# Kernel tuning notes

Measured on AMD Instinct MI355X. Metric: run time of the kernel, lower is better.

The kernel has to match this reference:

```python
import jax, jax.numpy as jnp
import numpy as np

B, T, D = 32, 2048, 128


def setup_inputs() -> dict:
    key = jax.random.key(0)
    k1, k2, k3 = jax.random.split(key, 3)
    values = jax.random.normal(k1, (B, T, D), dtype=jnp.float32)
    # monotonically increasing per-feature timestamps (irregular sampling)
    times = jnp.cumsum(jax.random.uniform(k2, (B, T, D), dtype=jnp.float32), axis=1)
    mask = jax.random.randint(k3, (B, T, D), 0, 2) > 0  # True = observed
    return {"values": values, "times": times, "mask": mask}


def _fill(x, t, mask):
    """Parallel forward fill (LOCF) and backward fill (NOCB) of x and t.

    Replaces the serial Keras RNN scan with cummax/cummin over observation
    indices followed by a gather. Matches ForwardCell semantics:
      forward : x init 0, t init times[:, 0, :]
      backward: x init 0, t init max(times, axis=1)
    """
    Tn = x.shape[1]
    ar = jnp.broadcast_to(jnp.arange(Tn, dtype=jnp.int32)[None, :, None], x.shape)
    # ---- forward fill ----
    fidx = jax.lax.cummax(jnp.where(mask, ar, -1), axis=1)  # last observed idx
    fvalid = fidx >= 0
    fi = jnp.clip(fidx, 0, Tn - 1)
    x_last = jnp.where(fvalid, jnp.take_along_axis(x, fi, axis=1), 0.0)
    t_last = jnp.where(fvalid, jnp.take_along_axis(t, fi, axis=1), t[:, :1, :])
    # ---- backward fill ----
    bidx = jax.lax.cummin(jnp.where(mask, ar, Tn), axis=1, reverse=True)  # next observed idx
    bvalid = bidx < Tn
    bi = jnp.clip(bidx, 0, Tn - 1)
    x_next = jnp.where(bvalid, jnp.take_along_axis(x, bi, axis=1), 0.0)
    t_next = jnp.where(bvalid, jnp.take_along_axis(t, bi, axis=1),
                       jnp.max(t, axis=1, keepdims=True))
    return x_last, t_last, x_next, t_next


def reference(values, times, mask):
    x_last, t_last, x_next, t_next = _fill(values, times, mask)
    denom = t_next - t_last
    num = x_last * (t_next - times) + x_next * (times - t_last)
    safe = denom != 0.0
    x_itp = num / jnp.where(safe, denom, 1.0)
    x_itp = jnp.where(safe & jnp.isfinite(x_itp), x_itp, 0.0)  # nan/inf -> 0
    return jnp.where(mask, values, x_itp)
```

## Files before the change

### kernel.cpp

```cpp
#include <hip/hip_runtime.h>
#include <math.h>

constexpr int B   = 32;
constexpr int T   = 2048;
constexpr int D   = 128;
constexpr int TB  = 32;
constexpr int W   = 8;
constexpr int RT  = TB + 2 * W;
constexpr int RG  = 8;
constexpr int RPT = RT / RG;
constexpr int DGN = 32;
constexpr int NT  = T / TB;

__global__ __launch_bounds__(256)
void linterp_kernel(const float* __restrict__ values,
                    const float* __restrict__ times,
                    const int*   __restrict__ mask,
                    float*       __restrict__ out)
{
    __shared__ float sFX[RG][D];
    __shared__ float sFT[RG][D];
    __shared__ float sBX[RG][D];
    __shared__ float sBT[RG][D];

    const int tid  = threadIdx.x;
    const int dg   = tid & (DGN - 1);
    const int rg   = tid >> 5;
    const int tile = blockIdx.x & (NT - 1);
    const int b    = blockIdx.x >> 6;
    const int d    = dg * 4;
    const int base = b * T * D + d;
    const int tlo  = tile * TB;
    const int row0 = tlo - W + rg * RPT;

    float4 v[RPT], tv[RPT];
    unsigned int mb[4] = {0u, 0u, 0u, 0u};
#pragma unroll
    for (int i = 0; i < RPT; ++i) {
        const int r = row0 + i;
        if (r >= 0 && r < T) {
            const int off = base + r * D;
            v[i]  = *(const float4*)(values + off);
            tv[i] = *(const float4*)(times + off);
            const int4 m = *(const int4*)(mask + off);
            mb[0] |= (m.x != 0 ? 1u : 0u) << i;
            mb[1] |= (m.y != 0 ? 1u : 0u) << i;
            mb[2] |= (m.z != 0 ? 1u : 0u) << i;
            mb[3] |= (m.w != 0 ? 1u : 0u) << i;
        } else {
            v[i]  = make_float4(0.f, 0.f, 0.f, 0.f);
            tv[i] = make_float4(0.f, 0.f, 0.f, 0.f);
        }
    }

    const float4 tf4 = *(const float4*)(times + base);
    const float4 te4 = *(const float4*)(times + base + (T - 1) * D);

    {
        float fX[4], fT[4], bX[4], bT[4];
#pragma unroll
        for (int j = 0; j < 4; ++j) { fX[j] = 0.f; fT[j] = -1.f; bX[j] = 0.f; bT[j] = -1.f; }
#pragma unroll
        for (int i = 0; i < RPT; ++i) {
            const float* xp = (const float*)&v[i];
            const float* tp = (const float*)&tv[i];
#pragma unroll
            for (int j = 0; j < 4; ++j) {
                if ((mb[j] >> i) & 1u) {
                    fX[j] = xp[j]; fT[j] = tp[j];
                    if (bT[j] < 0.f) { bX[j] = xp[j]; bT[j] = tp[j]; }
                }
            }
        }
        *(float4*)&sFX[rg][d] = make_float4(fX[0], fX[1], fX[2], fX[3]);
        *(float4*)&sFT[rg][d] = make_float4(fT[0], fT[1], fT[2], fT[3]);
        *(float4*)&sBX[rg][d] = make_float4(bX[0], bX[1], bX[2], bX[3]);
        *(float4*)&sBT[rg][d] = make_float4(bT[0], bT[1], bT[2], bT[3]);
    }
    __syncthreads();

    const bool has_out = (rg >= 1) && (rg <= 6);

    float cfX[4], cfT[4], cbX[4], cbT[4];
#pragma unroll
    for (int j = 0; j < 4; ++j) { cfX[j] = 0.f; cfT[j] = -1.f; cbX[j] = 0.f; cbT[j] = -1.f; }

    if (has_out) {
        for (int r2 = 0; r2 < rg; ++r2) {
            const float4 px = *(const float4*)&sFX[r2][d];
            const float4 pt = *(const float4*)&sFT[r2][d];
            const float* pxp = (const float*)&px;
            const float* ptp = (const float*)&pt;
#pragma unroll
            for (int j = 0; j < 4; ++j)
                if (ptp[j] >= 0.f) { cfX[j] = pxp[j]; cfT[j] = ptp[j]; }
        }
        for (int r2 = RG - 1; r2 > rg; --r2) {
            const float4 nx = *(const float4*)&sBX[r2][d];
            const float4 nt = *(const float4*)&sBT[r2][d];
            const float* nxp = (const float*)&nx;
            const float* ntp = (const float*)&nt;
#pragma unroll
            for (int j = 0; j < 4; ++j)
                if (ntp[j] >= 0.f) { cbX[j] = nxp[j]; cbT[j] = ntp[j]; }
        }

#pragma unroll
        for (int j = 0; j < 4; ++j) {
            if (cfT[j] < 0.f) {
                for (int r = tlo - W - 1; r >= 0; --r) {
                    const int off = base + r * D + j;
                    if (mask[off] != 0) { cfX[j] = values[off]; cfT[j] = times[off]; break; }
                }
                if (cfT[j] < 0.f) { cfX[j] = 0.f; cfT[j] = ((const float*)&tf4)[j]; }
            }
            if (cbT[j] < 0.f) {
                for (int r = tlo + TB + W; r < T; ++r) {
                    const int off = base + r * D + j;
                    if (mask[off] != 0) { cbX[j] = values[off]; cbT[j] = times[off]; break; }
                }
                if (cbT[j] < 0.f) { cbX[j] = 0.f; cbT[j] = ((const float*)&te4)[j]; }
            }
        }

        float4 tl[RPT];
#pragma unroll
        for (int i = 0; i < RPT; ++i) {
            float* xp = (float*)&v[i];
            const float* tp = (const float*)&tv[i];
            float* lp = (float*)&tl[i];
#pragma unroll
            for (int j = 0; j < 4; ++j) {
                if ((mb[j] >> i) & 1u) { cfX[j] = xp[j]; cfT[j] = tp[j]; }
                xp[j] = cfX[j];
                lp[j] = cfT[j];
            }
        }

#pragma unroll
        for (int i = RPT - 1; i >= 0; --i) {
            const int r = row0 + i;
            const float* xp = (const float*)&v[i];
            const float* tp = (const float*)&tv[i];
            const float* lp = (const float*)&tl[i];
            float4 o;
            float* op = (float*)&o;
#pragma unroll
            for (int j = 0; j < 4; ++j) {
                const bool obs = (mb[j] >> i) & 1u;
                if (obs) { cbX[j] = xp[j]; cbT[j] = tp[j]; }
                const float denom = cbT[j] - lp[j];
                const float num   = xp[j] * (cbT[j] - tp[j]) + cbX[j] * (tp[j] - lp[j]);
                const bool  safe  = (denom != 0.f);
                float xi = num / (safe ? denom : 1.f);
                xi = (safe && isfinite(xi)) ? xi : 0.f;
                op[j] = obs ? xp[j] : xi;
            }
            if (r >= tlo && r < tlo + TB)
                *(float4*)(out + base + r * D) = o;
        }
    }
}

extern "C" void kernel_launch(void* const* d_in, const int* in_sizes, int n_in,
                              void* d_out, int out_size, void* d_ws, size_t ws_size,
                              hipStream_t stream)
{
    const float* values = (const float*)d_in[0];
    const float* times  = (const float*)d_in[1];
    const int*   mask   = (const int*)d_in[2];
    float*       out    = (float*)d_out;

    linterp_kernel<<<B * NT, 256, 0, stream>>>(values, times, mask, out);
}
```

Before: 150.0 us.

## Stage values and mask tiles into LDS via direct global-to-LDS loads

Values and mask for each 48-row halo tile are now copied straight into shared memory with the global_load_lds builtin, and each thread reads its rows back from LDS. Times still go through registers. Out-of-range rows are clamped and then masked out as unobserved, and the first and last timestamps are read only in the rare fallback path. The aim is to cut VGPR pressure and issue overhead on the load path, at the cost of about 48KB of LDS per block, which may reduce occupancy.

```diff
diff --git a/kernel.cpp b/kernel.cpp
--- a/kernel.cpp
+++ b/kernel.cpp
@@ -9,8 +9,13 @@
 constexpr int RT  = TB + 2 * W;
 constexpr int RG  = 8;
 constexpr int RPT = RT / RG;
-constexpr int DGN = 32;
 constexpr int NT  = T / TB;
+constexpr int CHUNKS = RT * D * 4 / 1024;
+constexpr int CPW    = CHUNKS / 4;
+
+#define GL2LDS(g, l) __builtin_amdgcn_global_load_lds(                      \
+    (const __attribute__((address_space(1))) void*)(g),                     \
+    (__attribute__((address_space(3))) void*)(l), 16, 0, 0)
 
 __global__ __launch_bounds__(256)
 void linterp_kernel(const float* __restrict__ values,
@@ -18,51 +23,68 @@
                     const int*   __restrict__ mask,
                     float*       __restrict__ out)
 {
+    __shared__ float sV[RT * D];
+    __shared__ int   sM[RT * D];
     __shared__ float sFX[RG][D];
     __shared__ float sFT[RG][D];
     __shared__ float sBX[RG][D];
     __shared__ float sBT[RG][D];
 
     const int tid  = threadIdx.x;
-    const int dg   = tid & (DGN - 1);
+    const int dg   = tid & 31;
     const int rg   = tid >> 5;
     const int tile = blockIdx.x & (NT - 1);
     const int b    = blockIdx.x >> 6;
     const int d    = dg * 4;
-    const int base = b * T * D + d;
+    const int seqb = b * T * D;
+    const int base = seqb + d;
     const int tlo  = tile * TB;
     const int row0 = tlo - W + rg * RPT;
 
-    float4 v[RPT], tv[RPT];
-    unsigned int mb[4] = {0u, 0u, 0u, 0u};
+    {
+        const int lane     = tid & 63;
+        const int wv       = tid >> 6;
+        const int lrow_off = lane >> 5;
+        const int lcol     = (lane & 31) * 4;
 #pragma unroll
-    for (int i = 0; i < RPT; ++i) {
-        const int r = row0 + i;
-        if (r >= 0 && r < T) {
-            const int off = base + r * D;
-            v[i]  = *(const float4*)(values + off);
-            tv[i] = *(const float4*)(times + off);
-            const int4 m = *(const int4*)(mask + off);
-            mb[0] |= (m.x != 0 ? 1u : 0u) << i;
-            mb[1] |= (m.y != 0 ? 1u : 0u) << i;
-            mb[2] |= (m.z != 0 ? 1u : 0u) << i;
-            mb[3] |= (m.w != 0 ? 1u : 0u) << i;
-        } else {
-            v[i]  = make_float4(0.f, 0.f, 0.f, 0.f);
-            tv[i] = make_float4(0.f, 0.f, 0.f, 0.f);
+        for (int k = 0; k < CPW; ++k) {
+            const int c = wv * CPW + k;
+            int r = tlo - W + 2 * c + lrow_off;
+            r = min(max(r, 0), T - 1);
+            const int go = seqb + r * D + lcol;
+            GL2LDS(values + go, &sV[c * 256]);
+            GL2LDS(mask   + go, &sM[c * 256]);
         }
     }
 
-    const float4 tf4 = *(const float4*)(times + base);
-    const float4 te4 = *(const float4*)(times + base + (T - 1) * D);
+    float4 tv[RPT];
+#pragma unroll
+    for (int i = 0; i < RPT; ++i) {
+        int r = row0 + i;
+        r = min(max(r, 0), T - 1);
+        tv[i] = *(const float4*)(times + base + r * D);
+    }
 
+    __syncthreads();
+
+    float4 vv[RPT];
+    unsigned int mb[4] = {0u, 0u, 0u, 0u};
     {
         float fX[4], fT[4], bX[4], bT[4];
 #pragma unroll
         for (int j = 0; j < 4; ++j) { fX[j] = 0.f; fT[j] = -1.f; bX[j] = 0.f; bT[j] = -1.f; }
 #pragma unroll
         for (int i = 0; i < RPT; ++i) {
-            const float* xp = (const float*)&v[i];
+            const int lr = rg * RPT + i;
+            vv[i] = *(const float4*)&sV[lr * D + d];
+            const int4 m = *(const int4*)&sM[lr * D + d];
+            const int r = row0 + i;
+            const bool rv = (r >= 0) && (r < T);
+            mb[0] |= ((m.x != 0) && rv ? 1u : 0u) << i;
+            mb[1] |= ((m.y != 0) && rv ? 1u : 0u) << i;
+            mb[2] |= ((m.z != 0) && rv ? 1u : 0u) << i;
+            mb[3] |= ((m.w != 0) && rv ? 1u : 0u) << i;
+            const float* xp = (const float*)&vv[i];
             const float* tp = (const float*)&tv[i];
 #pragma unroll
             for (int j = 0; j < 4; ++j) {
@@ -79,13 +101,10 @@
     }
     __syncthreads();
 
-    const bool has_out = (rg >= 1) && (rg <= 6);
-
-    float cfX[4], cfT[4], cbX[4], cbT[4];
+    if (rg >= 1 && rg <= 6) {
+        float cfX[4], cfT[4], cbX[4], cbT[4];
 #pragma unroll
-    for (int j = 0; j < 4; ++j) { cfX[j] = 0.f; cfT[j] = -1.f; cbX[j] = 0.f; cbT[j] = -1.f; }
-
-    if (has_out) {
+        for (int j = 0; j < 4; ++j) { cfX[j] = 0.f; cfT[j] = -1.f; cbX[j] = 0.f; cbT[j] = -1.f; }
         for (int r2 = 0; r2 < rg; ++r2) {
             const float4 px = *(const float4*)&sFX[r2][d];
             const float4 pt = *(const float4*)&sFT[r2][d];
@@ -112,21 +131,21 @@
                     const int off = base + r * D + j;
                     if (mask[off] != 0) { cfX[j] = values[off]; cfT[j] = times[off]; break; }
                 }
-                if (cfT[j] < 0.f) { cfX[j] = 0.f; cfT[j] = ((const float*)&tf4)[j]; }
+                if (cfT[j] < 0.f) { cfX[j] = 0.f; cfT[j] = times[base + j]; }
             }
             if (cbT[j] < 0.f) {
                 for (int r = tlo + TB + W; r < T; ++r) {
                     const int off = base + r * D + j;
                     if (mask[off] != 0) { cbX[j] = values[off]; cbT[j] = times[off]; break; }
                 }
-                if (cbT[j] < 0.f) { cbX[j] = 0.f; cbT[j] = ((const float*)&te4)[j]; }
+                if (cbT[j] < 0.f) { cbX[j] = 0.f; cbT[j] = times[base + (T - 1) * D + j]; }
             }
         }
 
         float4 tl[RPT];
 #pragma unroll
         for (int i = 0; i < RPT; ++i) {
-            float* xp = (float*)&v[i];
+            float* xp = (float*)&vv[i];
             const float* tp = (const float*)&tv[i];
             float* lp = (float*)&tl[i];
 #pragma unroll
@@ -140,7 +159,7 @@
 #pragma unroll
         for (int i = RPT - 1; i >= 0; --i) {
             const int r = row0 + i;
-            const float* xp = (const float*)&v[i];
+            const float* xp = (const float*)&vv[i];
             const float* tp = (const float*)&tv[i];
             const float* lp = (const float*)&tl[i];
             float4 o;
```

Result: slower. 153.5 us (+2.4%).
